# Kernel tuning notes

Hardware: AMD Instinct MI355X
Metric: run time of the kernel (lower is better)

## Reference

```python
import jax, jax.numpy as jnp
import numpy as np

B, L, M, D = 8, 2048, 2048, 256


def setup_inputs() -> dict:
    key = jax.random.key(0)
    k1, k2, k3, k4, k5 = jax.random.split(key, 5)
    inp = jax.random.normal(k1, (B, L, D), dtype=jnp.float32)
    mem = jax.random.normal(k2, (B, M, D), dtype=jnp.float32)
    mask = jnp.ones((B, M), dtype=jnp.float32)
    # Learned parameters (Linear(D, 1, bias=False) -> weight vector of shape [D])
    w_input = jax.random.normal(k3, (D,), dtype=jnp.float32) / np.sqrt(D)
    w_memory = jax.random.normal(k4, (D,), dtype=jnp.float32) / np.sqrt(D)
    dot_scale = jax.random.uniform(k5, (D,), dtype=jnp.float32, minval=0.0, maxval=1.0 / np.sqrt(D))
    return {"input": inp, "memory": mem, "mask": mask,
            "w_input": w_input, "w_memory": w_memory, "dot_scale": dot_scale}


def reference(input, memory, mask, w_input, w_memory, dot_scale):
    # dropout with p=0.0 / eval mode -> identity
    input_dot = jnp.einsum('bld,d->bl', input, w_input)[:, :, None]      # [B, L, 1]
    memory_dot = jnp.einsum('bmd,d->bm', memory, w_memory)[:, None, :]   # [B, 1, M]
    cross_dot = jnp.einsum('bld,bmd->blm', input * dot_scale, memory)    # [B, L, M]
    att = input_dot + memory_dot + cross_dot                             # [B, L, M]
    att = att - 1e30 * (1.0 - mask[:, None, :])
    weight_one = jax.nn.softmax(att, axis=-1)                            # [B, L, M]
    output_one = jnp.einsum('blm,bmd->bld', weight_one, memory)          # [B, L, D]
    weight_two = jax.nn.softmax(jnp.max(att, axis=-1), axis=-1)[:, None, :]  # [B, 1, L]
    output_two = jnp.einsum('bol,bld->bod', weight_two, input)           # [B, 1, D]
    return jnp.concatenate(
        [input, output_one, input * output_one, output_two * output_one], axis=-1)
```

## Files before the change

### kernel.cpp

```cpp
#include <hip/hip_runtime.h>
#include <hip/hip_bf16.h>


typedef __bf16 bf16_t;
typedef bf16_t bf16x4 __attribute__((ext_vector_type(4)));
typedef bf16_t bf16x8 __attribute__((ext_vector_type(8)));
typedef float  f32x16 __attribute__((ext_vector_type(16)));

#define NB 8
#define NL 2048
#define NM 2048
#define ND 256
#define OUTW 1024
#define MT 64
#define MH 1024
#define NIT 16
#define LT 128
#define MEMT_X0 8388608u
#define FLASH_LDS 147456

__device__ __forceinline__ unsigned omap(unsigned x) {
    return ((x >> 10) << 12) | (x & 1023u);
}

__device__ __forceinline__ void dma16(const void* g, void* l) {
    __builtin_amdgcn_global_load_lds(
        (const __attribute__((address_space(1))) unsigned int*)g,
        (__attribute__((address_space(3))) unsigned int*)l, 16, 0, 0);
}

__global__ __launch_bounds__(256) void idot_kernel(
    const float* __restrict__ input, const float* __restrict__ w_input,
    float* __restrict__ ws_idot)
{
    int row  = blockIdx.x * 4 + (threadIdx.x >> 6);
    int lane = threadIdx.x & 63;
    float4 v  = *(const float4*)(input + (size_t)row * ND + lane * 4);
    float4 wv = *(const float4*)(w_input + lane * 4);
    float s = v.x * wv.x + v.y * wv.y + v.z * wv.z + v.w * wv.w;
    #pragma unroll
    for (int off = 1; off < 64; off <<= 1) s += __shfl_xor(s, off, 64);
    if (lane == 0) ws_idot[row] = s;
}

__global__ __launch_bounds__(256) void prep_kernel(
    const float* __restrict__ memory, const float* __restrict__ mask,
    const float* __restrict__ w_memory,
    float* __restrict__ ws_mbias, float* __restrict__ ws_numden,
    char* __restrict__ outc)
{
    __shared__ __align__(16) bf16_t lds[32 * 256];

    int b  = blockIdx.x >> 6;
    int mc = blockIdx.x & 63;
    int t  = threadIdx.x, w = t >> 6, lane = t & 63;

    if (blockIdx.x == 0) {
        for (int k = t; k < 2056; k += 256) ws_numden[k] = 0.f;
    }

    float4 wv = *(const float4*)(w_memory + lane * 4);

    #pragma unroll
    for (int it = 0; it < 8; ++it) {
        int rloc = it * 4 + w;
        int row  = b * NM + mc * 32 + rloc;
        float4 v = *(const float4*)(memory + (size_t)row * ND + lane * 4);
        float s = v.x * wv.x + v.y * wv.y + v.z * wv.z + v.w * wv.w;
        #pragma unroll
        for (int off = 1; off < 64; off <<= 1) s += __shfl_xor(s, off, 64);
        if (lane == 0) ws_mbias[row] = s - 1e30f * (1.0f - mask[row]);
        bf16x4 bv;
        bv[0] = (bf16_t)v.x; bv[1] = (bf16_t)v.y;
        bv[2] = (bf16_t)v.z; bv[3] = (bf16_t)v.w;
        unsigned x = 2u * ((unsigned)row * ND + lane * 4);
        *(bf16x4*)(outc + omap(x)) = bv;
        *(bf16x4*)(&lds[rloc * 256 + lane * 4]) = bv;
    }
    __syncthreads();
    int d = t;
    #pragma unroll
    for (int mc4 = 0; mc4 < 4; ++mc4) {
        bf16x8 pk;
        #pragma unroll
        for (int j = 0; j < 8; ++j) pk[j] = lds[(mc4 * 8 + j) * 256 + d];
        unsigned x = MEMT_X0 +
            2u * ((((unsigned)(b * 256 + mc * 4 + mc4)) * ND + d) * 8);
        *(bf16x8*)(outc + omap(x)) = pk;
    }
}

__global__ __launch_bounds__(512, 2) void flash_kernel(
    const float* __restrict__ input, const float* __restrict__ dot_scale,
    const float* __restrict__ ws_mbias, const char* __restrict__ outc,
    float* __restrict__ out, float* __restrict__ ws_l, float* __restrict__ ws_m)
{
    extern __shared__ __align__(16) char smem[];

    int bid = blockIdx.x;
    int half = bid & 1, b = (bid >> 1) & 7, lt = bid >> 4;
    int l0 = lt * LT;
    int m_base = half * MH;
    int t = threadIdx.x, w = t >> 6, lane = t & 63;
    int gw = w & 3, grp = w >> 2;
    int c = lane & 31, h = lane >> 5;

    const float* qrow = input + (size_t)(b * NL + l0 + gw * 32 + c) * ND;
    bf16x8 qf[16];
    #pragma unroll
    for (int ks = 0; ks < 16; ++ks) {
        int d0 = ks * 16 + h * 8;
        float4 a0 = *(const float4*)(qrow + d0);
        float4 a1 = *(const float4*)(qrow + d0 + 4);
        float4 s0 = *(const float4*)(dot_scale + d0);
        float4 s1 = *(const float4*)(dot_scale + d0 + 4);
        qf[ks][0] = (bf16_t)(a0.x * s0.x); qf[ks][1] = (bf16_t)(a0.y * s0.y);
        qf[ks][2] = (bf16_t)(a0.z * s0.z); qf[ks][3] = (bf16_t)(a0.w * s0.w);
        qf[ks][4] = (bf16_t)(a1.x * s1.x); qf[ks][5] = (bf16_t)(a1.y * s1.y);
        qf[ks][6] = (bf16_t)(a1.z * s1.z); qf[ks][7] = (bf16_t)(a1.w * s1.w);
    }

    unsigned xk = 2u * (((unsigned)(b * NM + m_base + grp * 32 + c)) * ND + h * 8);
    const char* kg = outc + omap(xk);
    unsigned xv = MEMT_X0 +
        2u * ((((unsigned)(b * 256 + (m_base >> 3) + grp * 4 + h)) * ND + c) * 8);
    const char* vg = outc + omap(xv);

    char* buf0 = smem;
    char* buf1 = smem + 65536;

    #define STAGE(nbuf) do {                                                  \
        _Pragma("unroll")                                                     \
        for (int j = 0; j < 4; ++j) {                                         \
            int i = gw * 4 + j;                                               \
            int ks = i >> 3, dt = i & 7;                                      \
            dma16(kg + i * 32, (nbuf) + grp * 16384 + i * 1024);              \
            dma16(vg + ks * 32768 + (dt >> 1) * 4096 + (dt & 1) * 512,        \
                  (nbuf) + 32768 + grp * 16384 + i * 1024);                   \
        }                                                                     \
        kg += 131072; vg += 131072; } while (0)

    STAGE(buf0);

    f32x16 oaccT[8];
    #pragma unroll
    for (int i = 0; i < 8; ++i)
        #pragma unroll
        for (int r = 0; r < 16; ++r) oaccT[i][r] = 0.f;
    float lsum = 0.f, mmax = -3e38f;

    const float* mb_base = ws_mbias + b * NM;
    bf16_t* pfw = (bf16_t*)(smem + 131072 + w * 2048);

    #pragma unroll 1
    for (int it = 0; it < NIT; ++it) {
        int m0 = m_base + it * MT + grp * 32;
        asm volatile("s_waitcnt vmcnt(0)" ::: "memory");
        __syncthreads();
        const char* cb = (it & 1) ? buf1 : buf0;
        char* nb = (it & 1) ? buf0 : buf1;
        const bf16_t* kb = (const bf16_t*)(cb + grp * 16384);
        const bf16_t* vb = (const bf16_t*)(cb + 32768 + grp * 16384);
        if (it + 1 < NIT) {
            STAGE(nb);
        }
        float mv = mb_base[m0 + c];
        f32x16 S;
        #pragma unroll
        for (int r = 0; r < 16; ++r) S[r] = 0.f;
        #pragma unroll
        for (int ks = 0; ks < 16; ++ks) {
            bf16x8 k0 = *(const bf16x8*)(kb + ks * 512 + lane * 8);
            S = __builtin_amdgcn_mfma_f32_32x32x16_bf16(k0, qf[ks], S, 0, 0, 0);
        }
        #pragma unroll
        for (int j2 = 0; j2 < 4; ++j2) {
            bf16x4 pk;
            #pragma unroll
            for (int q = 0; q < 4; ++q) {
                int r = j2 * 4 + q;
                float v = S[r] + __shfl(mv, (r & 3) + 8 * (r >> 2) + 4 * h, 64);
                mmax = fmaxf(mmax, v);
                float e = __expf(v);
                lsum += e;
                pk[q] = (bf16_t)e;
            }
            *(bf16x4*)(pfw + j2 * 256 + c * 8 + h * 4) = pk;
        }
        asm volatile("s_waitcnt lgkmcnt(0)" ::: "memory");
        #pragma unroll
        for (int ks = 0; ks < 2; ++ks) {
            bf16x8 pb = *(const bf16x8*)(pfw + ks * 512 + lane * 8);
            #pragma unroll
            for (int dt = 0; dt < 8; ++dt) {
                bf16x8 vv = *(const bf16x8*)(vb + (ks * 8 + dt) * 512 + lane * 8);
                oaccT[dt] = __builtin_amdgcn_mfma_f32_32x32x16_bf16(vv, pb, oaccT[dt], 0, 0, 0);
            }
        }
    }
    #undef STAGE

    __syncthreads();
    if (grp == 1) {
        float* dst = (float*)(smem + gw * 32768);
        #pragma unroll
        for (int dt = 0; dt < 8; ++dt) {
            #pragma unroll
            for (int q = 0; q < 4; ++q) {
                float4 v4;
                v4.x = oaccT[dt][q * 4 + 0]; v4.y = oaccT[dt][q * 4 + 1];
                v4.z = oaccT[dt][q * 4 + 2]; v4.w = oaccT[dt][q * 4 + 3];
                *(float4*)(dst + dt * 1024 + q * 256 + lane * 4) = v4;
            }
        }
        float* aux = (float*)(smem + 131072 + gw * 2048);
        aux[lane] = lsum;
        aux[64 + lane] = mmax;
    }
    __syncthreads();
    if (grp == 0) {
        const float* src = (const float*)(smem + gw * 32768);
        #pragma unroll
        for (int dt = 0; dt < 8; ++dt) {
            #pragma unroll
            for (int q = 0; q < 4; ++q) {
                float4 v4 = *(const float4*)(src + dt * 1024 + q * 256 + lane * 4);
                oaccT[dt][q * 4 + 0] += v4.x; oaccT[dt][q * 4 + 1] += v4.y;
                oaccT[dt][q * 4 + 2] += v4.z; oaccT[dt][q * 4 + 3] += v4.w;
            }
        }
        const float* aux = (const float*)(smem + 131072 + gw * 2048);
        lsum += aux[lane];
        mmax = fmaxf(mmax, aux[64 + lane]);
    }
    __syncthreads();
    if (grp == 0) {
        mmax = fmaxf(mmax, __shfl_xor(mmax, 32, 64));
        lsum += __shfl_xor(lsum, 32, 64);
        if (lane < 32) {
            int row = b * NL + l0 + gw * 32 + lane;
            ws_l[half * (NB * NL) + row] = lsum;
            ws_m[half * (NB * NL) + row] = mmax;
        }
        float* patch = (float*)(smem + gw * 4352);
        float* oseg = out + (size_t)(b * NL + l0 + gw * 32) * OUTW + ND * (1 + half);
        #pragma unroll
        for (int dt = 0; dt < 8; ++dt) {
            asm volatile("s_waitcnt lgkmcnt(0)" ::: "memory");
            #pragma unroll
            for (int r = 0; r < 16; ++r)
                patch[((r & 3) + 8 * (r >> 2) + 4 * h) * 33 + c] = oaccT[dt][r];
            asm volatile("s_waitcnt lgkmcnt(0)" ::: "memory");
            #pragma unroll
            for (int rr = 0; rr < 16; ++rr) {
                float val = patch[c * 33 + rr * 2 + h];
                oseg[(size_t)(rr * 2 + h) * OUTW + dt * 32 + c] = val;
            }
        }
    }
}

__global__ __launch_bounds__(256) void o2_kernel(
    const float* __restrict__ input, const float* __restrict__ ws_idot,
    const float* __restrict__ ws_m, float* __restrict__ ws_num,
    float* __restrict__ ws_den)
{
    __shared__ float4 red[256];
    int b = blockIdx.x >> 5, slice = blockIdx.x & 31;
    int t = threadIdx.x;
    int lgrp = t >> 6, d4 = (t & 63) * 4;
    float4 acc = {0.f, 0.f, 0.f, 0.f};
    float esum = 0.f;
    for (int i = 0; i < 16; ++i) {
        int row = b * NL + slice * 64 + lgrp * 16 + i;
        float e = __expf(ws_idot[row] + fmaxf(ws_m[row], ws_m[NB * NL + row]));
        float4 v = *(const float4*)(input + (size_t)row * ND + d4);
        acc.x += e * v.x; acc.y += e * v.y;
        acc.z += e * v.z; acc.w += e * v.w;
        esum += e;
    }
    red[t] = acc;
    __syncthreads();
    if (t < 64) {
        float4 a0 = red[t], a1 = red[t + 64], a2 = red[t + 128], a3 = red[t + 192];
        float* dst = ws_num + b * ND + t * 4;
        atomicAdd(dst + 0, a0.x + a1.x + a2.x + a3.x);
        atomicAdd(dst + 1, a0.y + a1.y + a2.y + a3.y);
        atomicAdd(dst + 2, a0.z + a1.z + a2.z + a3.z);
        atomicAdd(dst + 3, a0.w + a1.w + a2.w + a3.w);
    }
    if ((t & 63) == 0) atomicAdd(ws_den + b, esum);
}

__global__ __launch_bounds__(256) void assembly_kernel(
    const float* __restrict__ input, const float* __restrict__ ws_num,
    const float* __restrict__ ws_den, const float* __restrict__ ws_l,
    float* __restrict__ out)
{
    size_t tid = (size_t)blockIdx.x * 256 + threadIdx.x;
    size_t row = tid >> 6;
    int d = (int)(tid & 63) * 4;
    int b = (int)(row >> 11);
    float inv  = 1.0f / (ws_l[row] + ws_l[NB * NL + row]);
    float dinv = 1.0f / ws_den[b];
    float* po = out + row * OUTW;
    float4 in = *(const float4*)(input + row * ND + d);
    float4 pa = *(const float4*)(po + ND + d);
    float4 pb = *(const float4*)(po + 2 * ND + d);
    float4 nu = *(const float4*)(ws_num + b * ND + d);
    float4 o1;
    o1.x = (pa.x + pb.x) * inv; o1.y = (pa.y + pb.y) * inv;
    o1.z = (pa.z + pb.z) * inv; o1.w = (pa.w + pb.w) * inv;
    float4 o2v;
    o2v.x = nu.x * dinv; o2v.y = nu.y * dinv;
    o2v.z = nu.z * dinv; o2v.w = nu.w * dinv;
    *(float4*)(po + d) = in;
    *(float4*)(po + ND + d) = o1;
    float4 q;
    q.x = in.x * o1.x; q.y = in.y * o1.y; q.z = in.z * o1.z; q.w = in.w * o1.w;
    *(float4*)(po + 2 * ND + d) = q;
    float4 r;
    r.x = o2v.x * o1.x; r.y = o2v.y * o1.y; r.z = o2v.z * o1.z; r.w = o2v.w * o1.w;
    *(float4*)(po + 3 * ND + d) = r;
}

extern "C" void kernel_launch(void* const* d_in, const int* in_sizes, int n_in,
                              void* d_out, int out_size, void* d_ws, size_t ws_size,
                              hipStream_t stream) {
    const float* input     = (const float*)d_in[0];
    const float* memory    = (const float*)d_in[1];
    const float* mask      = (const float*)d_in[2];
    const float* w_input   = (const float*)d_in[3];
    const float* w_memory  = (const float*)d_in[4];
    const float* dot_scale = (const float*)d_in[5];
    float* out = (float*)d_out;
    char* outc = (char*)d_out;
    float* ws  = (float*)d_ws;

    float* ws_idot  = ws;
    float* ws_mbias = ws + 16384;
    float* ws_l     = ws + 32768;
    float* ws_m     = ws + 65536;
    float* ws_num   = ws + 98304;
    float* ws_den   = ws + 100352;

    idot_kernel<<<4096, 256, 0, stream>>>(input, w_input, ws_idot);
    prep_kernel<<<512, 256, 0, stream>>>(memory, mask, w_memory, ws_mbias,
                                         ws_num, outc);
    flash_kernel<<<256, 512, FLASH_LDS, stream>>>(input, dot_scale, ws_mbias,
                                                  outc, out, ws_l, ws_m);
    o2_kernel<<<256, 256, 0, stream>>>(input, ws_idot, ws_m, ws_num, ws_den);
    assembly_kernel<<<4096, 256, 0, stream>>>(input, ws_num, ws_den, ws_l, out);
}
```

Before: 199.5 us.

## Fuse input-dot into flash kernel and pass P via lane shuffles instead of LDS

Removes the separate idot kernel by computing the input·w_input dot product inside the flash kernel's Q-load loop for one half of the blocks. Replaces the LDS round-trip for the bf16 softmax probabilities with register cross-lane shuffles that build the B operand directly. Loads the memory bias as vector float4s instead of per-element shuffles, and raises wave priority around the MFMA sections. LDS footprint shrinks because the P staging buffer is gone. The trade-off is extra register pressure and some imbalance, since only part of the blocks do the idot work.

```diff
diff --git a/kernel.cpp b/kernel.cpp
--- a/kernel.cpp
+++ b/kernel.cpp
@@ -6,6 +6,8 @@
 typedef bf16_t bf16x4 __attribute__((ext_vector_type(4)));
 typedef bf16_t bf16x8 __attribute__((ext_vector_type(8)));
 typedef float  f32x16 __attribute__((ext_vector_type(16)));
+typedef unsigned int u32x2 __attribute__((ext_vector_type(2)));
+typedef unsigned int u32x4 __attribute__((ext_vector_type(4)));
 
 #define NB 8
 #define NL 2048
@@ -17,7 +19,7 @@
 #define NIT 16
 #define LT 128
 #define MEMT_X0 8388608u
-#define FLASH_LDS 147456
+#define FLASH_LDS 133120
 
 __device__ __forceinline__ unsigned omap(unsigned x) {
     return ((x >> 10) << 12) | (x & 1023u);
@@ -27,20 +29,6 @@
     __builtin_amdgcn_global_load_lds(
         (const __attribute__((address_space(1))) unsigned int*)g,
         (__attribute__((address_space(3))) unsigned int*)l, 16, 0, 0);
-}
-
-__global__ __launch_bounds__(256) void idot_kernel(
-    const float* __restrict__ input, const float* __restrict__ w_input,
-    float* __restrict__ ws_idot)
-{
-    int row  = blockIdx.x * 4 + (threadIdx.x >> 6);
-    int lane = threadIdx.x & 63;
-    float4 v  = *(const float4*)(input + (size_t)row * ND + lane * 4);
-    float4 wv = *(const float4*)(w_input + lane * 4);
-    float s = v.x * wv.x + v.y * wv.y + v.z * wv.z + v.w * wv.w;
-    #pragma unroll
-    for (int off = 1; off < 64; off <<= 1) s += __shfl_xor(s, off, 64);
-    if (lane == 0) ws_idot[row] = s;
 }
 
 __global__ __launch_bounds__(256) void prep_kernel(
@@ -92,8 +80,10 @@
 
 __global__ __launch_bounds__(512, 2) void flash_kernel(
     const float* __restrict__ input, const float* __restrict__ dot_scale,
-    const float* __restrict__ ws_mbias, const char* __restrict__ outc,
-    float* __restrict__ out, float* __restrict__ ws_l, float* __restrict__ ws_m)
+    const float* __restrict__ w_input, const float* __restrict__ ws_mbias,
+    const char* __restrict__ outc, float* __restrict__ out,
+    float* __restrict__ ws_l, float* __restrict__ ws_m,
+    float* __restrict__ ws_idot)
 {
     extern __shared__ __align__(16) char smem[];
 
@@ -106,6 +96,8 @@
     int c = lane & 31, h = lane >> 5;
 
     const float* qrow = input + (size_t)(b * NL + l0 + gw * 32 + c) * ND;
+    bool do_idot = (half == 0) && (grp == 0);
+    float idot_s = 0.f;
     bf16x8 qf[16];
     #pragma unroll
     for (int ks = 0; ks < 16; ++ks) {
@@ -114,10 +106,20 @@
         float4 a1 = *(const float4*)(qrow + d0 + 4);
         float4 s0 = *(const float4*)(dot_scale + d0);
         float4 s1 = *(const float4*)(dot_scale + d0 + 4);
+        if (do_idot) {
+            float4 w0 = *(const float4*)(w_input + d0);
+            float4 w1 = *(const float4*)(w_input + d0 + 4);
+            idot_s += a0.x * w0.x + a0.y * w0.y + a0.z * w0.z + a0.w * w0.w
+                    + a1.x * w1.x + a1.y * w1.y + a1.z * w1.z + a1.w * w1.w;
+        }
         qf[ks][0] = (bf16_t)(a0.x * s0.x); qf[ks][1] = (bf16_t)(a0.y * s0.y);
         qf[ks][2] = (bf16_t)(a0.z * s0.z); qf[ks][3] = (bf16_t)(a0.w * s0.w);
         qf[ks][4] = (bf16_t)(a1.x * s1.x); qf[ks][5] = (bf16_t)(a1.y * s1.y);
         qf[ks][6] = (bf16_t)(a1.z * s1.z); qf[ks][7] = (bf16_t)(a1.w * s1.w);
+    }
+    if (do_idot) {
+        idot_s += __shfl_xor(idot_s, 32, 64);
+        if (lane < 32) ws_idot[b * NL + l0 + gw * 32 + lane] = idot_s;
     }
 
     unsigned xk = 2u * (((unsigned)(b * NM + m_base + grp * 32 + c)) * ND + h * 8);
@@ -150,7 +152,6 @@
     float lsum = 0.f, mmax = -3e38f;
 
     const float* mb_base = ws_mbias + b * NM;
-    bf16_t* pfw = (bf16_t*)(smem + 131072 + w * 2048);
 
     #pragma unroll 1
     for (int it = 0; it < NIT; ++it) {
@@ -164,38 +165,60 @@
         if (it + 1 < NIT) {
             STAGE(nb);
         }
-        float mv = mb_base[m0 + c];
+        const float* mrow = mb_base + m0 + 4 * h;
+        float4 mbv0 = *(const float4*)(mrow);
+        float4 mbv1 = *(const float4*)(mrow + 8);
+        float4 mbv2 = *(const float4*)(mrow + 16);
+        float4 mbv3 = *(const float4*)(mrow + 24);
         f32x16 S;
         #pragma unroll
         for (int r = 0; r < 16; ++r) S[r] = 0.f;
+        __builtin_amdgcn_s_setprio(1);
         #pragma unroll
         for (int ks = 0; ks < 16; ++ks) {
             bf16x8 k0 = *(const bf16x8*)(kb + ks * 512 + lane * 8);
             S = __builtin_amdgcn_mfma_f32_32x32x16_bf16(k0, qf[ks], S, 0, 0, 0);
         }
-        #pragma unroll
-        for (int j2 = 0; j2 < 4; ++j2) {
-            bf16x4 pk;
+        __builtin_amdgcn_s_setprio(0);
+        u32x2 own[4];
+        #pragma unroll
+        for (int g = 0; g < 4; ++g) {
+            float4 mbv = (g == 0) ? mbv0 : (g == 1) ? mbv1 : (g == 2) ? mbv2 : mbv3;
+            bf16x4 tq;
             #pragma unroll
             for (int q = 0; q < 4; ++q) {
-                int r = j2 * 4 + q;
-                float v = S[r] + __shfl(mv, (r & 3) + 8 * (r >> 2) + 4 * h, 64);
+                float v = S[g * 4 + q] +
+                          ((q == 0) ? mbv.x : (q == 1) ? mbv.y : (q == 2) ? mbv.z : mbv.w);
                 mmax = fmaxf(mmax, v);
                 float e = __expf(v);
                 lsum += e;
-                pk[q] = (bf16_t)e;
-            }
-            *(bf16x4*)(pfw + j2 * 256 + c * 8 + h * 4) = pk;
-        }
-        asm volatile("s_waitcnt lgkmcnt(0)" ::: "memory");
+                tq[q] = (bf16_t)e;
+            }
+            own[g] = __builtin_bit_cast(u32x2, tq);
+        }
         #pragma unroll
         for (int ks = 0; ks < 2; ++ks) {
-            bf16x8 pb = *(const bf16x8*)(pfw + ks * 512 + lane * 8);
+            unsigned oAlo = own[2 * ks].x,     oAhi = own[2 * ks].y;
+            unsigned oBlo = own[2 * ks + 1].x, oBhi = own[2 * ks + 1].y;
+            unsigned slo = h ? oAlo : oBlo;
+            unsigned shi = h ? oAhi : oBhi;
+            unsigned rlo = (unsigned)__shfl_xor((int)slo, 32, 64);
+            unsigned rhi = (unsigned)__shfl_xor((int)shi, 32, 64);
+            unsigned mlo = h ? oBlo : oAlo;
+            unsigned mhi = h ? oBhi : oAhi;
+            u32x4 uu;
+            uu.x = h ? rlo : mlo;
+            uu.y = h ? rhi : mhi;
+            uu.z = h ? mlo : rlo;
+            uu.w = h ? mhi : rhi;
+            bf16x8 pb = __builtin_bit_cast(bf16x8, uu);
+            __builtin_amdgcn_s_setprio(1);
             #pragma unroll
             for (int dt = 0; dt < 8; ++dt) {
                 bf16x8 vv = *(const bf16x8*)(vb + (ks * 8 + dt) * 512 + lane * 8);
                 oaccT[dt] = __builtin_amdgcn_mfma_f32_32x32x16_bf16(vv, pb, oaccT[dt], 0, 0, 0);
             }
+            __builtin_amdgcn_s_setprio(0);
         }
     }
     #undef STAGE
@@ -213,7 +236,7 @@
                 *(float4*)(dst + dt * 1024 + q * 256 + lane * 4) = v4;
             }
         }
-        float* aux = (float*)(smem + 131072 + gw * 2048);
+        float* aux = (float*)(smem + 131072 + gw * 512);
         aux[lane] = lsum;
         aux[64 + lane] = mmax;
     }
@@ -229,7 +252,7 @@
                 oaccT[dt][q * 4 + 2] += v4.z; oaccT[dt][q * 4 + 3] += v4.w;
             }
         }
-        const float* aux = (const float*)(smem + 131072 + gw * 2048);
+        const float* aux = (const float*)(smem + 131072 + gw * 512);
         lsum += aux[lane];
         mmax = fmaxf(mmax, aux[64 + lane]);
     }
@@ -344,11 +367,11 @@
     float* ws_num   = ws + 98304;
     float* ws_den   = ws + 100352;
 
-    idot_kernel<<<4096, 256, 0, stream>>>(input, w_input, ws_idot);
     prep_kernel<<<512, 256, 0, stream>>>(memory, mask, w_memory, ws_mbias,
                                          ws_num, outc);
-    flash_kernel<<<256, 512, FLASH_LDS, stream>>>(input, dot_scale, ws_mbias,
-                                                  outc, out, ws_l, ws_m);
+    flash_kernel<<<256, 512, FLASH_LDS, stream>>>(input, dot_scale, w_input,
+                                                  ws_mbias, outc, out,
+                                                  ws_l, ws_m, ws_idot);
     o2_kernel<<<256, 256, 0, stream>>>(input, ws_idot, ws_m, ws_num, ws_den);
     assembly_kernel<<<4096, 256, 0, stream>>>(input, ws_num, ws_den, ws_l, out);
 }
```

After: 194.8 us. -2.4%, faster.
